# Kernel optimization log

Measured on AMD Instinct MI355X. Metric: run time of the kernel, lower is better.

## Reference

```python
import jax, jax.numpy as jnp
import numpy as np

D, L, DIM, G = 64, 64, 512, 256      # dialogues, utterances/dialogue, feat dim, graph dim
TOPK_FRAC = 0.2
TAU = 0.07


def setup_inputs() -> dict:
    key = jax.random.key(0)
    ks = jax.random.split(key, 7)
    N = D * L
    t = jax.random.normal(ks[0], (N, DIM), dtype=jnp.float32)
    a = jax.random.normal(ks[1], (N, DIM), dtype=jnp.float32)
    v = jax.random.normal(ks[2], (N, DIM), dtype=jnp.float32)
    W_fc = jax.random.normal(ks[3], (DIM, G), dtype=jnp.float32) / np.sqrt(DIM)
    b_fc = jnp.zeros((G,), dtype=jnp.float32)
    W_h = jax.random.normal(ks[4], (G, G), dtype=jnp.float32) / np.sqrt(G)
    b_h = jnp.zeros((G,), dtype=jnp.float32)
    dia_len = np.full((D,), L, dtype=np.int64)  # uniform dialogue lengths
    return {"t": t, "a": a, "v": v, "W_fc": W_fc, "b_fc": b_fc,
            "W_h": W_h, "b_h": b_h, "dia_len": dia_len}


def _contrastive_loss(x, y, tau=TAU):
    # symmetric InfoNCE with matched-index positives
    xn = x / (jnp.linalg.norm(x, axis=-1, keepdims=True) + 1e-8)
    yn = y / (jnp.linalg.norm(y, axis=-1, keepdims=True) + 1e-8)
    sim = (xn @ yn.T) / tau                     # [N, N]
    pos_xy = jnp.diagonal(jax.nn.log_softmax(sim, axis=1))
    pos_yx = jnp.diagonal(jax.nn.log_softmax(sim, axis=0))
    return -(pos_xy.mean() + pos_yx.mean()) / 2.0


def _forward(t, a, v, W_fc, b_fc, W_h, b_h, dia_len):
    dl = np.asarray(dia_len)
    d, l = dl.shape[0], int(dl[0])              # uniform lengths assumed
    m = 3 * l                                   # nodes (and hyperedges) per dialogue
    k = int(l * TOPK_FRAC)
    dim = t.shape[-1]

    # per-dialogue node features in original order [t_i; a_i; v_i]
    feat = jnp.concatenate([t.reshape(d, l, dim),
                            a.reshape(d, l, dim),
                            v.reshape(d, l, dim)], axis=1)   # [d, m, dim]

    # squared euclidean distances (same ordering as torch.cdist for top-k smallest)
    sq = jnp.sum(feat * feat, axis=-1)                        # [d, m]
    d2 = sq[:, :, None] + sq[:, None, :] - 2.0 * jnp.einsum('dmf,dnf->dmn', feat, feat)
    d2 = jax.lax.stop_gradient(jnp.maximum(d2, 0.0))
    _, idx = jax.lax.top_k(-d2, k)                            # [d, m, k] nearest nodes

    # boolean incidence H[d, e, n] = node n participates in hyperedge e
    # (set-union dedup in the original == boolean OR here)
    node_ids = jnp.arange(m)
    H_nb = (idx[..., None] == node_ids).any(axis=2)           # [d, m, m]
    u = node_ids // 3                                         # central utterance of edge j
    cent = ((node_ids[None, :] == u[:, None]) |
            (node_ids[None, :] == u[:, None] + l) |
            (node_ids[None, :] == u[:, None] + 2 * l))        # [m, m]
    H = (H_nb | cent[None]).astype(feat.dtype)                # [d, m, m]

    # fc projection
    X = feat @ W_fc + b_fc                                    # [d, m, G]

    # hypergraph conv: node -> hyperedge (mean) -> node (mean), then Linear+ReLU
    deg_e = H.sum(axis=2, keepdims=True)                      # [d, m, 1]
    E = jnp.einsum('den,dng->deg', H, X) / deg_e              # edge features
    deg_v = H.sum(axis=1)[..., None]                          # [d, m, 1]
    Y = jnp.einsum('den,deg->dng', H, E) / deg_v              # node features
    out = jax.nn.relu(Y @ W_h + b_h)                          # [d, m, G]

    # reverse_features: regroup by modality across dialogues
    tn = out[:, :l].reshape(d * l, -1)
    an = out[:, l:2 * l].reshape(d * l, -1)
    vn = out[:, 2 * l:].reshape(d * l, -1)
    out_cat = jnp.concatenate([tn, an, vn], axis=1)           # [N, 3G]

    loss = (_contrastive_loss(tn, an) + _contrastive_loss(tn, vn)
            + _contrastive_loss(an, vn)) / 3.0
    return out_cat, loss


def reference(t, a, v, W_fc, b_fc, W_h, b_h, dia_len):
    return _forward(t, a, v, W_fc, b_fc, W_h, b_h, dia_len)
```

## Files before the change

### kernel.cpp

```cpp
#include <hip/hip_runtime.h>
#include <math.h>

#define NDIAL 64
#define M3    192
#define DIMF  512
#define GDIM  256
#define NROW  4096
#define TOPK  12
#define INV_TAU (1.0f/0.07f)

typedef __attribute__((ext_vector_type(8))) short bf16x8;
typedef __attribute__((ext_vector_type(4))) float f32x4;
typedef __attribute__((ext_vector_type(8))) ushort us8;
typedef _Float16 f16x8 __attribute__((ext_vector_type(8)));
typedef _Float16 f16x4v __attribute__((ext_vector_type(4)));
typedef __attribute__((address_space(3))) ushort lds_us;
typedef const __attribute__((address_space(1))) ushort gm_us;

__device__ __forceinline__ ushort f2bf(float f) {
    unsigned u = __float_as_uint(f);
    unsigned r = (u + 0x7fff + ((u >> 16) & 1)) >> 16;
    return (ushort)r;
}

template<int KDIM>
__device__ __forceinline__ void mm64bt(
    const float* __restrict__ A, int lda,
    const float* __restrict__ B, int ldb,
    float acc[4][4])
{
    __shared__ float As[64][33];
    __shared__ float Bs[32][68];
    const int tid = threadIdx.x;
    const int tx = tid & 15, ty = tid >> 4;

#pragma unroll
    for (int r = 0; r < 4; r++)
#pragma unroll
        for (int c = 0; c < 4; c++) acc[r][c] = 0.f;

    for (int k0 = 0; k0 < KDIM; k0 += 32) {
#pragma unroll
        for (int i = 0; i < 2; i++) {
            int f = tid + i * 256;
            int m = f >> 3, k4 = f & 7;
            const float4 v4 = *(const float4*)(A + (size_t)m * lda + k0 + k4 * 4);
            As[m][k4 * 4 + 0] = v4.x;
            As[m][k4 * 4 + 1] = v4.y;
            As[m][k4 * 4 + 2] = v4.z;
            As[m][k4 * 4 + 3] = v4.w;
        }
#pragma unroll
        for (int i = 0; i < 2; i++) {
            int f = tid + i * 256;
            int n = f >> 3, k4 = f & 7;
            const float4 v4 = *(const float4*)(B + (size_t)n * ldb + k0 + k4 * 4);
            Bs[k4 * 4 + 0][n] = v4.x;
            Bs[k4 * 4 + 1][n] = v4.y;
            Bs[k4 * 4 + 2][n] = v4.z;
            Bs[k4 * 4 + 3][n] = v4.w;
        }
        __syncthreads();
#pragma unroll
        for (int kk = 0; kk < 32; kk++) {
            float4 b = *(const float4*)&Bs[kk][tx * 4];
#pragma unroll
            for (int r = 0; r < 4; r++) {
                float av = As[ty * 4 + r][kk];
                acc[r][0] += av * b.x;
                acc[r][1] += av * b.y;
                acc[r][2] += av * b.z;
                acc[r][3] += av * b.w;
            }
        }
        __syncthreads();
    }
}

template<int KD, int NW>
__device__ __forceinline__ void hgemm_bt(const _Float16* __restrict__ A, int lda,
                                         const _Float16* __restrict__ B, int ldb,
                                         f32x4 acc[4][4]) {
    __shared__ __align__(16) _Float16 As[64 * 40];
    __shared__ __align__(16) _Float16 Bs[NW * 64 * 40];
    const int tid = threadIdx.x;
    const int lane = tid & 63, w = tid >> 6;
    const int qd = lane >> 4, l15 = lane & 15;

#pragma unroll
    for (int fm = 0; fm < 4; fm++)
#pragma unroll
        for (int fn = 0; fn < 4; fn++)
            acc[fm][fn] = (f32x4){0.f, 0.f, 0.f, 0.f};

    for (int k0 = 0; k0 < KD; k0 += 32) {
        for (int f = tid; f < 256; f += NW * 64) {
            int row = f >> 2, c8 = f & 3;
            *(float4*)&As[row * 40 + c8 * 8] =
                *(const float4*)&A[(size_t)row * lda + k0 + c8 * 8];
        }
#pragma unroll
        for (int i = 0; i < 4; i++) {
            int f = tid + i * NW * 64;
            int row = f >> 2, c8 = f & 3;
            *(float4*)&Bs[row * 40 + c8 * 8] =
                *(const float4*)&B[(size_t)row * ldb + k0 + c8 * 8];
        }
        __syncthreads();
        f16x8 af[4], bfr[4];
#pragma unroll
        for (int fm = 0; fm < 4; fm++)
            af[fm] = *(const f16x8*)&As[(fm * 16 + l15) * 40 + qd * 8];
#pragma unroll
        for (int fn = 0; fn < 4; fn++)
            bfr[fn] = *(const f16x8*)&Bs[(w * 64 + fn * 16 + l15) * 40 + qd * 8];
#pragma unroll
        for (int fm = 0; fm < 4; fm++)
#pragma unroll
            for (int fn = 0; fn < 4; fn++)
                acc[fm][fn] = __builtin_amdgcn_mfma_f32_16x16x32_f16(
                    af[fm], bfr[fn], acc[fm][fn], 0, 0, 0);
        __syncthreads();
    }
}

__device__ __forceinline__ const float* node_ptr(const float* t, const float* a,
                                                 const float* v, int d, int j) {
    int mod = j >> 6, i = j & 63;
    const float* base = (mod == 0) ? t : (mod == 1) ? a : v;
    return base + (size_t)(d * 64 + i) * DIMF;
}

__global__ void kprep(const float* __restrict__ t, const float* __restrict__ a,
                      const float* __restrict__ v, const float* __restrict__ Wfc,
                      const float* __restrict__ Wh, _Float16* __restrict__ featb,
                      _Float16* __restrict__ WfcT, _Float16* __restrict__ WhT,
                      float* __restrict__ sq, float* __restrict__ rs,
                      float* __restrict__ cs, float* __restrict__ degV,
                      _Float16* __restrict__ HbT) {
    int b = blockIdx.x, tid = threadIdx.x;
    if (b < 6144) {
        int e = (b * 256 + tid) * 4;
        int d = e / (M3 * DIMF);
        int rem = e % (M3 * DIMF);
        int n = rem / DIMF, kk = rem % DIMF;
        int mod = n >> 6, i = n & 63;
        const float* src = ((mod == 0) ? t : (mod == 1) ? a : v)
                           + (size_t)(d * 64 + i) * DIMF + kk;
        float4 x = *(const float4*)src;
        f16x4v o = {(_Float16)x.x, (_Float16)x.y, (_Float16)x.z, (_Float16)x.w};
        *(f16x4v*)&featb[e] = o;
    } else if (b < 6272) {
        int e = ((b - 6144) * 256 + tid) * 4;
        int g = e >> 9, kk = e & 511;
        f16x4v o = {(_Float16)Wfc[(size_t)(kk + 0) * GDIM + g],
                    (_Float16)Wfc[(size_t)(kk + 1) * GDIM + g],
                    (_Float16)Wfc[(size_t)(kk + 2) * GDIM + g],
                    (_Float16)Wfc[(size_t)(kk + 3) * GDIM + g]};
        *(f16x4v*)&WfcT[(size_t)g * DIMF + kk] = o;
    } else if (b < 6336) {
        int e = ((b - 6272) * 256 + tid) * 4;
        int go = e >> 8, g = e & 255;
        f16x4v o = {(_Float16)Wh[(size_t)(g + 0) * GDIM + go],
                    (_Float16)Wh[(size_t)(g + 1) * GDIM + go],
                    (_Float16)Wh[(size_t)(g + 2) * GDIM + go],
                    (_Float16)Wh[(size_t)(g + 3) * GDIM + go]};
        *(f16x4v*)&WhT[(size_t)go * GDIM + g] = o;
    } else if (b < 9408) {
        int lane = tid & 63, wv = tid >> 6;
        int n = (b - 6336) * 4 + wv;
        int d = n / M3, j = n % M3;
        const float4* s4 = (const float4*)node_ptr(t, a, v, d, j);
        float s = 0.f;
#pragma unroll
        for (int q = 0; q < 2; q++) {
            float4 x = s4[lane + q * 64];
            s += x.x * x.x + x.y * x.y + x.z * x.z + x.w * x.w;
        }
        for (int o = 32; o; o >>= 1) s += __shfl_down(s, o);
        if (lane == 0) sq[n] = s;
    } else if (b < 9456) {
        int i = (b - 9408) * 256 + tid;
        rs[i] = 0.f; cs[i] = 0.f; degV[i] = 0.f;
    } else {
        int i = (b - 9456) * 256 + tid;
        ulonglong2 z = {0ull, 0ull};
        *(ulonglong2*)&HbT[(size_t)i * 8] = z;
    }
}

__global__ void k1_d2(const float* __restrict__ t, const float* __restrict__ a,
                      const float* __restrict__ v, const float* __restrict__ sq,
                      float* __restrict__ d2) {
    int tileid = blockIdx.x;
    int d = blockIdx.y;
    int bi = (tileid < 3) ? 0 : (tileid < 5) ? 1 : 2;
    int bj = (tileid < 3) ? tileid : (tileid < 5) ? tileid - 2 : 2;
    const float* A = ((bi == 0) ? t : (bi == 1) ? a : v) + (size_t)d * 64 * DIMF;
    const float* B = ((bj == 0) ? t : (bj == 1) ? a : v) + (size_t)d * 64 * DIMF;
    float acc[4][4];
    mm64bt<DIMF>(A, DIMF, B, DIMF, acc);
    int tx = threadIdx.x & 15, ty = threadIdx.x >> 4;
    const float* sqd = sq + d * M3;
    float* outp = d2 + (size_t)d * M3 * M3;
#pragma unroll
    for (int r = 0; r < 4; r++)
#pragma unroll
        for (int c = 0; c < 4; c++) {
            int il = bi * 64 + ty * 4 + r;
            int jl = bj * 64 + tx * 4 + c;
            float vv = fmaxf(sqd[il] + sqd[jl] - 2.f * acc[r][c], 0.f);
            outp[(size_t)il * M3 + jl] = vv;
            if (bi != bj) outp[(size_t)jl * M3 + il] = vv;
        }
}

__global__ void k2_topk(const float* __restrict__ d2, _Float16* __restrict__ Hb,
                        _Float16* __restrict__ HbT, float* __restrict__ degE,
                        float* __restrict__ degV) {
    int lane = threadIdx.x & 63, wv = threadIdx.x >> 6;
    int r = blockIdx.x * 4 + wv;
    int d = r / M3, e = r % M3;
    const float* row = d2 + (size_t)r * M3;
    float w0 = row[lane], w1 = row[lane + 64], w2 = row[lane + 128];
    bool s0 = false, s1 = false, s2 = false;
#pragma unroll
    for (int it = 0; it < TOPK; it++) {
        float bv = w0; int bi = lane;
        if (w1 < bv) { bv = w1; bi = lane + 64; }
        if (w2 < bv) { bv = w2; bi = lane + 128; }
#pragma unroll
        for (int o = 1; o < 64; o <<= 1) {
            float ov = __shfl_xor(bv, o);
            int   oi = __shfl_xor(bi, o);
            if (ov < bv || (ov == bv && oi < bi)) { bv = ov; bi = oi; }
        }
        if (bi == lane)            { s0 = true; w0 = 3.4e38f; }
        else if (bi == lane + 64)  { s1 = true; w1 = 3.4e38f; }
        else if (bi == lane + 128) { s2 = true; w2 = 3.4e38f; }
    }
    int u = e / 3;
    if (lane == u) { s0 = true; s1 = true; s2 = true; }
    float f0 = s0 ? 1.f : 0.f, f1 = s1 ? 1.f : 0.f, f2 = s2 ? 1.f : 0.f;
    _Float16* Hrow = Hb + (size_t)r * M3;
    Hrow[lane] = (_Float16)f0;
    Hrow[lane + 64] = (_Float16)f1;
    Hrow[lane + 128] = (_Float16)f2;
    float cnt = f0 + f1 + f2;
#pragma unroll
    for (int o = 1; o < 64; o <<= 1) cnt += __shfl_xor(cnt, o);
    if (lane == 0) degE[r] = cnt;
    float* dv = degV + d * M3;
    _Float16* HT = HbT + (size_t)d * M3 * M3;
    if (s0) { atomicAdd(&dv[lane], 1.f);       HT[(size_t)lane * M3 + e] = (_Float16)1.f; }
    if (s1) { atomicAdd(&dv[lane + 64], 1.f);  HT[(size_t)(lane + 64) * M3 + e] = (_Float16)1.f; }
    if (s2) { atomicAdd(&dv[lane + 128], 1.f); HT[(size_t)(lane + 128) * M3 + e] = (_Float16)1.f; }
}

__global__ void k3_x(const _Float16* __restrict__ WfcT, const _Float16* __restrict__ featb,
                     const float* __restrict__ bfc, _Float16* __restrict__ XT) {
    int gb = blockIdx.x, d = blockIdx.y;
    const _Float16* A = WfcT + (size_t)gb * 64 * DIMF;
    const _Float16* B = featb + (size_t)d * M3 * DIMF;
    f32x4 acc[4][4];
    hgemm_bt<DIMF, 3>(A, DIMF, B, DIMF, acc);
    int lane = threadIdx.x & 63, w = threadIdx.x >> 6;
    int qd = lane >> 4, l15 = lane & 15;
    _Float16* out = XT + (size_t)d * GDIM * M3;
#pragma unroll
    for (int fm = 0; fm < 4; fm++)
#pragma unroll
        for (int rg = 0; rg < 4; rg++) {
            int g = gb * 64 + fm * 16 + qd * 4 + rg;
            float bias = bfc[g];
#pragma unroll
            for (int fn = 0; fn < 4; fn++) {
                int n = w * 64 + fn * 16 + l15;
                out[(size_t)g * M3 + n] = (_Float16)(acc[fm][fn][rg] + bias);
            }
        }
}

__global__ void k4_E(const _Float16* __restrict__ XT, const _Float16* __restrict__ Hb,
                     const float* __restrict__ degE, _Float16* __restrict__ ET) {
    int gb = blockIdx.x, d = blockIdx.y;
    const _Float16* A = XT + (size_t)d * GDIM * M3 + (size_t)gb * 64 * M3;
    const _Float16* B = Hb + (size_t)d * M3 * M3;
    f32x4 acc[4][4];
    hgemm_bt<M3, 3>(A, M3, B, M3, acc);
    int lane = threadIdx.x & 63, w = threadIdx.x >> 6;
    int qd = lane >> 4, l15 = lane & 15;
    float ide[4];
#pragma unroll
    for (int fn = 0; fn < 4; fn++)
        ide[fn] = 1.f / degE[d * M3 + w * 64 + fn * 16 + l15];
    _Float16* out = ET + (size_t)d * GDIM * M3;
#pragma unroll
    for (int fm = 0; fm < 4; fm++)
#pragma unroll
        for (int rg = 0; rg < 4; rg++) {
            int g = gb * 64 + fm * 16 + qd * 4 + rg;
#pragma unroll
            for (int fn = 0; fn < 4; fn++) {
                int e = w * 64 + fn * 16 + l15;
                out[(size_t)g * M3 + e] = (_Float16)(acc[fm][fn][rg] * ide[fn]);
            }
        }
}

__global__ void k5_Y(const _Float16* __restrict__ HbT, const _Float16* __restrict__ ET,
                     const float* __restrict__ degV, _Float16* __restrict__ Y) {
    int nb = blockIdx.x, d = blockIdx.y;
    const _Float16* A = HbT + (size_t)d * M3 * M3 + (size_t)nb * 64 * M3;
    const _Float16* B = ET + (size_t)d * GDIM * M3;
    f32x4 acc[4][4];
    hgemm_bt<M3, 4>(A, M3, B, M3, acc);
    int lane = threadIdx.x & 63, w = threadIdx.x >> 6;
    int qd = lane >> 4, l15 = lane & 15;
    _Float16* out = Y + ((size_t)d * M3 + nb * 64) * GDIM;
#pragma unroll
    for (int fm = 0; fm < 4; fm++)
#pragma unroll
        for (int rg = 0; rg < 4; rg++) {
            int ml = fm * 16 + qd * 4 + rg;
            float idv = 1.f / degV[d * M3 + nb * 64 + ml];
#pragma unroll
            for (int fn = 0; fn < 4; fn++) {
                int g = w * 64 + fn * 16 + l15;
                out[(size_t)ml * GDIM + g] = (_Float16)(acc[fm][fn][rg] * idv);
            }
        }
}

__global__ __launch_bounds__(256) void k6_out(const _Float16* __restrict__ Y,
                                              const _Float16* __restrict__ WhT,
                                              const float* __restrict__ bh,
                                              float* __restrict__ outp,
                                              ushort* __restrict__ xnb) {
    __shared__ float tile[64 * 256];
    __shared__ float ssq[64];
    int b = blockIdx.x, tid = threadIdx.x;
    if (tid < 64) ssq[tid] = 0.f;
    const _Float16* A = Y + (size_t)b * 64 * GDIM;
    f32x4 acc[4][4];
    hgemm_bt<GDIM, 4>(A, GDIM, WhT, GDIM, acc);
    int lane = tid & 63, w = tid >> 6;
    int qd = lane >> 4, l15 = lane & 15;
    int d = b / 3, mod = b % 3;
    float bb[4];
#pragma unroll
    for (int fn = 0; fn < 4; fn++)
        bb[fn] = bh[w * 64 + fn * 16 + l15];
#pragma unroll
    for (int fm = 0; fm < 4; fm++)
#pragma unroll
        for (int rg = 0; rg < 4; rg++) {
            int i = fm * 16 + qd * 4 + rg;
            float* orow = outp + (size_t)(d * 64 + i) * 768 + mod * GDIM;
            float s2 = 0.f;
#pragma unroll
            for (int fn = 0; fn < 4; fn++) {
                int go = w * 64 + fn * 16 + l15;
                float vv = fmaxf(acc[fm][fn][rg] + bb[fn], 0.f);
                orow[go] = vv;
                tile[i * 256 + go] = vv;
                s2 += vv * vv;
            }
            s2 += __shfl_xor(s2, 1);
            s2 += __shfl_xor(s2, 2);
            s2 += __shfl_xor(s2, 4);
            s2 += __shfl_xor(s2, 8);
            if (l15 == 0) atomicAdd(&ssq[i], s2);
        }
    __syncthreads();
    if (tid < 64) ssq[tid] = 1.f / (sqrtf(ssq[tid]) + 1e-8f);
    __syncthreads();
#pragma unroll
    for (int it = 0; it < 8; it++) {
        int f = tid + it * 256;
        int row = f >> 5, c = f & 31;
        float4 xa = *(const float4*)&tile[row * 256 + c * 8];
        float4 xb = *(const float4*)&tile[row * 256 + c * 8 + 4];
        float iv = ssq[row];
        us8 o = {f2bf(xa.x * iv), f2bf(xa.y * iv), f2bf(xa.z * iv), f2bf(xa.w * iv),
                 f2bf(xb.x * iv), f2bf(xb.y * iv), f2bf(xb.z * iv), f2bf(xb.w * iv)};
        int rx = d * 64 + row;
        int slot = (c & 24) | ((c & 7) ^ (row & 7));
        *(us8*)&xnb[((size_t)mod * NROW + rx) * GDIM + slot * 8] = o;
    }
}

#define TILE9 128
#define STAGE9(ELT)                                                        \
    {                                                                      \
        __builtin_amdgcn_global_load_lds(pa0 + (ELT), la0, 16, 0, 0);      \
        __builtin_amdgcn_global_load_lds(pb0 + (ELT), lb0, 16, 0, 0);      \
        __builtin_amdgcn_global_load_lds(pa1 + (ELT), la1, 16, 0, 0);      \
        __builtin_amdgcn_global_load_lds(pb1 + (ELT), lb1, 16, 0, 0);      \
        __builtin_amdgcn_global_load_lds(pa2 + (ELT), la2, 16, 0, 0);      \
        __builtin_amdgcn_global_load_lds(pb2 + (ELT), lb2, 16, 0, 0);      \
        __builtin_amdgcn_global_load_lds(pa3 + (ELT), la3, 16, 0, 0);      \
        __builtin_amdgcn_global_load_lds(pb3 + (ELT), lb3, 16, 0, 0);      \
    }
__global__ __launch_bounds__(256, 4) void k9_mfma(const ushort* __restrict__ xnb,
                                                  float* __restrict__ rs,
                                                  float* __restrict__ cs,
                                                  float* __restrict__ diag) {
    int lin = blockIdx.x + (blockIdx.y << 5) + (blockIdx.z << 10);
    int vid = (lin >> 3) + (lin & 7) * 384;
    int p  = vid >> 10;
    int r0 = vid & 1023;
    int ci = r0 >> 5, cj = r0 & 31;
    int px = (p == 2) ? 1 : 0;
    int py = (p == 0) ? 1 : 2;
    const ushort* A = xnb + ((size_t)px * NROW + ci * TILE9) * GDIM;
    const ushort* B = xnb + ((size_t)py * NROW + cj * TILE9) * GDIM;

    __shared__ __align__(16) ushort As[TILE9 * 64];
    __shared__ __align__(16) ushort Bs[TILE9 * 64];

    const int tid = threadIdx.x;
    const int lane = tid & 63, w = tid >> 6;
    const int wrow = w >> 1, wcol = w & 1;
    const int qd = lane >> 4, l15 = lane & 15;
    const int lrow = lane >> 3, lslot = lane & 7;

    const int rbase = w * 32 + lrow;
    const int cbase = lslot * 8;
    const gm_us* pa0 = (gm_us*)(A + (size_t)(rbase +  0) * GDIM + cbase);
    const gm_us* pa1 = (gm_us*)(A + (size_t)(rbase +  8) * GDIM + cbase);
    const gm_us* pa2 = (gm_us*)(A + (size_t)(rbase + 16) * GDIM + cbase);
    const gm_us* pa3 = (gm_us*)(A + (size_t)(rbase + 24) * GDIM + cbase);
    const gm_us* pb0 = (gm_us*)(B + (size_t)(rbase +  0) * GDIM + cbase);
    const gm_us* pb1 = (gm_us*)(B + (size_t)(rbase +  8) * GDIM + cbase);
    const gm_us* pb2 = (gm_us*)(B + (size_t)(rbase + 16) * GDIM + cbase);
    const gm_us* pb3 = (gm_us*)(B + (size_t)(rbase + 24) * GDIM + cbase);
    lds_us* la0 = (lds_us*)&As[(w * 32 +  0) * 64];
    lds_us* la1 = (lds_us*)&As[(w * 32 +  8) * 64];
    lds_us* la2 = (lds_us*)&As[(w * 32 + 16) * 64];
    lds_us* la3 = (lds_us*)&As[(w * 32 + 24) * 64];
    lds_us* lb0 = (lds_us*)&Bs[(w * 32 +  0) * 64];
    lds_us* lb1 = (lds_us*)&Bs[(w * 32 +  8) * 64];
    lds_us* lb2 = (lds_us*)&Bs[(w * 32 + 16) * 64];
    lds_us* lb3 = (lds_us*)&Bs[(w * 32 + 24) * 64];

    f32x4 acc[4][4] = {};

    auto compute = [&]() {
#pragma unroll
        for (int kk = 0; kk < 2; kk++) {
            bf16x8 af[4], bfv[4];
#pragma unroll
            for (int fm = 0; fm < 4; fm++) {
                int ar = wrow * 64 + fm * 16 + l15;
                af[fm] = *(const bf16x8*)&As[ar * 64 + ((kk * 4 + qd) ^ (ar & 7)) * 8];
            }
#pragma unroll
            for (int fn = 0; fn < 4; fn++) {
                int br = wcol * 64 + fn * 16 + l15;
                bfv[fn] = *(const bf16x8*)&Bs[br * 64 + ((kk * 4 + qd) ^ (br & 7)) * 8];
            }
#pragma unroll
            for (int fm = 0; fm < 4; fm++)
#pragma unroll
                for (int fn = 0; fn < 4; fn++)
                    acc[fm][fn] = __builtin_amdgcn_mfma_f32_16x16x32_bf16(
                        af[fm], bfv[fn], acc[fm][fn], 0, 0, 0);
        }
    };

    STAGE9(0);   __syncthreads(); compute(); __syncthreads();
    STAGE9(64);  __syncthreads(); compute(); __syncthreads();
    STAGE9(128); __syncthreads(); compute(); __syncthreads();
    STAGE9(192); __syncthreads(); compute(); __syncthreads();

    const float C2 = INV_TAU * 1.44269504088896f;
    f32x4 rv[4] = {};
    f32x4 cv[4] = {};
#pragma unroll
    for (int fm = 0; fm < 4; fm++)
#pragma unroll
        for (int fn = 0; fn < 4; fn++) {
            f32x4 sv = acc[fm][fn] * C2;
            f32x4 ev;
#pragma unroll
            for (int rg = 0; rg < 4; rg++)
                ev[rg] = exp2f(sv[rg]);
            rv[fm] += ev;
            cv[fn] += ev;
        }
    if (ci == cj) {
#pragma unroll
        for (int fm = 0; fm < 4; fm++)
#pragma unroll
            for (int fn = 0; fn < 4; fn++)
#pragma unroll
                for (int rg = 0; rg < 4; rg++) {
                    int lr = wrow * 64 + fm * 16 + qd * 4 + rg;
                    int lc = wcol * 64 + fn * 16 + l15;
                    if (lr == lc)
                        diag[p * NROW + ci * TILE9 + lr] = acc[fm][fn][rg] * INV_TAU;
                }
    }
#pragma unroll
    for (int fm = 0; fm < 4; fm++)
#pragma unroll
        for (int rg = 0; rg < 4; rg++) {
            float s = rv[fm][rg];
            s += __shfl_xor(s, 1);
            s += __shfl_xor(s, 2);
            s += __shfl_xor(s, 4);
            s += __shfl_xor(s, 8);
            if (l15 == 0)
                atomicAdd(&rs[p * NROW + ci * TILE9 + wrow * 64 + fm * 16 + qd * 4 + rg], s);
        }
#pragma unroll
    for (int fn = 0; fn < 4; fn++) {
        float s = (cv[fn][0] + cv[fn][1]) + (cv[fn][2] + cv[fn][3]);
        s += __shfl_xor(s, 16);
        s += __shfl_xor(s, 32);
        if (qd == 0)
            atomicAdd(&cs[p * NROW + cj * TILE9 + wcol * 64 + fn * 16 + l15], s);
    }
}

__global__ void k10_loss(const float* __restrict__ diag, const float* __restrict__ rs,
                         const float* __restrict__ cs, float* __restrict__ outp) {
    float acc = 0.f;
    for (int i = threadIdx.x; i < 3 * NROW; i += 256)
        acc += 2.f * diag[i] - logf(rs[i]) - logf(cs[i]);
    int lane = threadIdx.x & 63, wv = threadIdx.x >> 6;
    for (int o = 32; o; o >>= 1) acc += __shfl_down(acc, o);
    __shared__ float red[4];
    if (lane == 0) red[wv] = acc;
    __syncthreads();
    if (threadIdx.x == 0) {
        float tot = red[0] + red[1] + red[2] + red[3];
        outp[(size_t)NROW * 768] = -tot / (NROW * 6.0f);
    }
}

extern "C" void kernel_launch(void* const* d_in, const int* in_sizes, int n_in,
                              void* d_out, int out_size, void* d_ws, size_t ws_size,
                              hipStream_t stream) {
    const float* t   = (const float*)d_in[0];
    const float* a   = (const float*)d_in[1];
    const float* v   = (const float*)d_in[2];
    const float* Wfc = (const float*)d_in[3];
    const float* bfc = (const float*)d_in[4];
    const float* Wh  = (const float*)d_in[5];
    const float* bh  = (const float*)d_in[6];
    float* outp = (float*)d_out;
    float* ws = (float*)d_ws;

    float* sq    = ws;
    float* d2    = sq + 12288;
    float* HbF   = d2 + 2359296;
    float* HbTF  = HbF + 1179648;
    float* degE  = HbTF + 1179648;
    float* degV  = degE + 12288;
    float* featF = degV + 12288;
    float* WfcTF = featF + 3145728;
    float* WhTF  = WfcTF + 65536;
    float* XTF   = WhTF + 32768;
    float* ETF   = XTF + 1572864;
    float* YF    = ETF + 1572864;
    float* rs    = YF + 1572864;
    float* cs    = rs + 12288;
    float* diag  = cs + 12288;

    _Float16* Hb    = (_Float16*)HbF;
    _Float16* HbT   = (_Float16*)HbTF;
    _Float16* featb = (_Float16*)featF;
    _Float16* WfcT  = (_Float16*)WfcTF;
    _Float16* WhT   = (_Float16*)WhTF;
    _Float16* XT    = (_Float16*)XTF;
    _Float16* ET    = (_Float16*)ETF;
    _Float16* Y     = (_Float16*)YF;
    ushort*   xnb   = (ushort*)d2;

    kprep  <<<10608, 256, 0, stream>>>(t, a, v, Wfc, Wh, featb, WfcT, WhT,
                                       sq, rs, cs, degV, HbT);
    k1_d2  <<<dim3(6, 64), 256, 0, stream>>>(t, a, v, sq, d2);
    k2_topk<<<3072, 256, 0, stream>>>(d2, Hb, HbT, degE, degV);
    k3_x   <<<dim3(4, 64), 192, 0, stream>>>(WfcT, featb, bfc, XT);
    k4_E   <<<dim3(4, 64), 192, 0, stream>>>(XT, Hb, degE, ET);
    k5_Y   <<<dim3(3, 64), 256, 0, stream>>>(HbT, ET, degV, Y);
    k6_out <<<192, 256, 0, stream>>>(Y, WhT, bh, outp, xnb);
    k9_mfma<<<dim3(32, 32, 3), 256, 0, stream>>>(xnb, rs, cs, diag);
    k10_loss<<<1, 256, 0, stream>>>(diag, rs, cs, outp);
}
```

Baseline: 284.6 us.

## Compute pairwise distance Gram matrix with split-fp16 MFMA instead of FP32 FMA

Replaces the scalar FP32 tiled GEMM in the distance kernel with MFMA fp16 matrix instructions. Each feature is split into a high and a low fp16 part in the prep kernel, and four MFMA products recover near-FP32 precision for the top-k selection. This removes the slow FP32 SIMD inner loop. In exchange it adds an extra fp16 residual buffer, aliased onto the XT scratch region, and extra writes in the prep kernel.

```diff
diff --git a/kernel.cpp b/kernel.cpp
--- a/kernel.cpp
+++ b/kernel.cpp
@@ -21,60 +21,6 @@
     unsigned u = __float_as_uint(f);
     unsigned r = (u + 0x7fff + ((u >> 16) & 1)) >> 16;
     return (ushort)r;
-}
-
-template<int KDIM>
-__device__ __forceinline__ void mm64bt(
-    const float* __restrict__ A, int lda,
-    const float* __restrict__ B, int ldb,
-    float acc[4][4])
-{
-    __shared__ float As[64][33];
-    __shared__ float Bs[32][68];
-    const int tid = threadIdx.x;
-    const int tx = tid & 15, ty = tid >> 4;
-
-#pragma unroll
-    for (int r = 0; r < 4; r++)
-#pragma unroll
-        for (int c = 0; c < 4; c++) acc[r][c] = 0.f;
-
-    for (int k0 = 0; k0 < KDIM; k0 += 32) {
-#pragma unroll
-        for (int i = 0; i < 2; i++) {
-            int f = tid + i * 256;
-            int m = f >> 3, k4 = f & 7;
-            const float4 v4 = *(const float4*)(A + (size_t)m * lda + k0 + k4 * 4);
-            As[m][k4 * 4 + 0] = v4.x;
-            As[m][k4 * 4 + 1] = v4.y;
-            As[m][k4 * 4 + 2] = v4.z;
-            As[m][k4 * 4 + 3] = v4.w;
-        }
-#pragma unroll
-        for (int i = 0; i < 2; i++) {
-            int f = tid + i * 256;
-            int n = f >> 3, k4 = f & 7;
-            const float4 v4 = *(const float4*)(B + (size_t)n * ldb + k0 + k4 * 4);
-            Bs[k4 * 4 + 0][n] = v4.x;
-            Bs[k4 * 4 + 1][n] = v4.y;
-            Bs[k4 * 4 + 2][n] = v4.z;
-            Bs[k4 * 4 + 3][n] = v4.w;
-        }
-        __syncthreads();
-#pragma unroll
-        for (int kk = 0; kk < 32; kk++) {
-            float4 b = *(const float4*)&Bs[kk][tx * 4];
-#pragma unroll
-            for (int r = 0; r < 4; r++) {
-                float av = As[ty * 4 + r][kk];
-                acc[r][0] += av * b.x;
-                acc[r][1] += av * b.y;
-                acc[r][2] += av * b.z;
-                acc[r][3] += av * b.w;
-            }
-        }
-        __syncthreads();
-    }
 }
 
 template<int KD, int NW>
@@ -134,7 +80,8 @@
 __global__ void kprep(const float* __restrict__ t, const float* __restrict__ a,
                       const float* __restrict__ v, const float* __restrict__ Wfc,
                       const float* __restrict__ Wh, _Float16* __restrict__ featb,
-                      _Float16* __restrict__ WfcT, _Float16* __restrict__ WhT,
+                      _Float16* __restrict__ featlo, _Float16* __restrict__ WfcT,
+                      _Float16* __restrict__ WhT,
                       float* __restrict__ sq, float* __restrict__ rs,
                       float* __restrict__ cs, float* __restrict__ degV,
                       _Float16* __restrict__ HbT) {
@@ -148,8 +95,13 @@
         const float* src = ((mod == 0) ? t : (mod == 1) ? a : v)
                            + (size_t)(d * 64 + i) * DIMF + kk;
         float4 x = *(const float4*)src;
-        f16x4v o = {(_Float16)x.x, (_Float16)x.y, (_Float16)x.z, (_Float16)x.w};
+        _Float16 h0 = (_Float16)x.x, h1 = (_Float16)x.y;
+        _Float16 h2 = (_Float16)x.z, h3 = (_Float16)x.w;
+        f16x4v o = {h0, h1, h2, h3};
         *(f16x4v*)&featb[e] = o;
+        f16x4v ol = {(_Float16)(x.x - (float)h0), (_Float16)(x.y - (float)h1),
+                     (_Float16)(x.z - (float)h2), (_Float16)(x.w - (float)h3)};
+        *(f16x4v*)&featlo[e] = ol;
     } else if (b < 6272) {
         int e = ((b - 6144) * 256 + tid) * 4;
         int g = e >> 9, kk = e & 511;
@@ -189,27 +141,60 @@
     }
 }
 
-__global__ void k1_d2(const float* __restrict__ t, const float* __restrict__ a,
-                      const float* __restrict__ v, const float* __restrict__ sq,
+__global__ __launch_bounds__(256) void k1_d2(const _Float16* __restrict__ featb,
+                      const _Float16* __restrict__ featlo,
+                      const float* __restrict__ sq,
                       float* __restrict__ d2) {
     int tileid = blockIdx.x;
     int d = blockIdx.y;
     int bi = (tileid < 3) ? 0 : (tileid < 5) ? 1 : 2;
     int bj = (tileid < 3) ? tileid : (tileid < 5) ? tileid - 2 : 2;
-    const float* A = ((bi == 0) ? t : (bi == 1) ? a : v) + (size_t)d * 64 * DIMF;
-    const float* B = ((bj == 0) ? t : (bj == 1) ? a : v) + (size_t)d * 64 * DIMF;
-    float acc[4][4];
-    mm64bt<DIMF>(A, DIMF, B, DIMF, acc);
-    int tx = threadIdx.x & 15, ty = threadIdx.x >> 4;
+    const size_t base = (size_t)d * M3 * DIMF;
+    const _Float16* Ah = featb  + base + (size_t)bi * 64 * DIMF;
+    const _Float16* Al = featlo + base + (size_t)bi * 64 * DIMF;
+    const _Float16* Bh = featb  + base + (size_t)bj * 64 * DIMF;
+    const _Float16* Bl = featlo + base + (size_t)bj * 64 * DIMF;
+
+    __shared__ __align__(16) _Float16 Ahs[64 * 40], Als[64 * 40];
+    __shared__ __align__(16) _Float16 Bhs[64 * 40], Bls[64 * 40];
+    const int tid = threadIdx.x;
+    const int lane = tid & 63, w = tid >> 6;
+    const int qd = lane >> 4, l15 = lane & 15;
+
+    f32x4 acc[4];
+#pragma unroll
+    for (int fm = 0; fm < 4; fm++) acc[fm] = (f32x4){0.f, 0.f, 0.f, 0.f};
+
+    for (int k0 = 0; k0 < DIMF; k0 += 32) {
+        int row = tid >> 2, c8 = tid & 3;
+        *(float4*)&Ahs[row * 40 + c8 * 8] = *(const float4*)&Ah[(size_t)row * DIMF + k0 + c8 * 8];
+        *(float4*)&Als[row * 40 + c8 * 8] = *(const float4*)&Al[(size_t)row * DIMF + k0 + c8 * 8];
+        *(float4*)&Bhs[row * 40 + c8 * 8] = *(const float4*)&Bh[(size_t)row * DIMF + k0 + c8 * 8];
+        *(float4*)&Bls[row * 40 + c8 * 8] = *(const float4*)&Bl[(size_t)row * DIMF + k0 + c8 * 8];
+        __syncthreads();
+        f16x8 bh = *(const f16x8*)&Bhs[(w * 16 + l15) * 40 + qd * 8];
+        f16x8 bl = *(const f16x8*)&Bls[(w * 16 + l15) * 40 + qd * 8];
+#pragma unroll
+        for (int fm = 0; fm < 4; fm++) {
+            f16x8 ah = *(const f16x8*)&Ahs[(fm * 16 + l15) * 40 + qd * 8];
+            f16x8 al = *(const f16x8*)&Als[(fm * 16 + l15) * 40 + qd * 8];
+            acc[fm] = __builtin_amdgcn_mfma_f32_16x16x32_f16(ah, bh, acc[fm], 0, 0, 0);
+            acc[fm] = __builtin_amdgcn_mfma_f32_16x16x32_f16(ah, bl, acc[fm], 0, 0, 0);
+            acc[fm] = __builtin_amdgcn_mfma_f32_16x16x32_f16(al, bh, acc[fm], 0, 0, 0);
+            acc[fm] = __builtin_amdgcn_mfma_f32_16x16x32_f16(al, bl, acc[fm], 0, 0, 0);
+        }
+        __syncthreads();
+    }
+
     const float* sqd = sq + d * M3;
     float* outp = d2 + (size_t)d * M3 * M3;
 #pragma unroll
-    for (int r = 0; r < 4; r++)
-#pragma unroll
-        for (int c = 0; c < 4; c++) {
-            int il = bi * 64 + ty * 4 + r;
-            int jl = bj * 64 + tx * 4 + c;
-            float vv = fmaxf(sqd[il] + sqd[jl] - 2.f * acc[r][c], 0.f);
+    for (int fm = 0; fm < 4; fm++)
+#pragma unroll
+        for (int rg = 0; rg < 4; rg++) {
+            int il = bi * 64 + fm * 16 + qd * 4 + rg;
+            int jl = bj * 64 + w * 16 + l15;
+            float vv = fmaxf(sqd[il] + sqd[jl] - 2.f * acc[fm][rg], 0.f);
             outp[(size_t)il * M3 + jl] = vv;
             if (bi != bj) outp[(size_t)jl * M3 + il] = vv;
         }
@@ -578,10 +563,11 @@
     _Float16* ET    = (_Float16*)ETF;
     _Float16* Y     = (_Float16*)YF;
     ushort*   xnb   = (ushort*)d2;
-
-    kprep  <<<10608, 256, 0, stream>>>(t, a, v, Wfc, Wh, featb, WfcT, WhT,
-                                       sq, rs, cs, degV, HbT);
-    k1_d2  <<<dim3(6, 64), 256, 0, stream>>>(t, a, v, sq, d2);
+    _Float16* featlo = (_Float16*)XTF;
+
+    kprep  <<<10608, 256, 0, stream>>>(t, a, v, Wfc, Wh, featb, featlo, WfcT,
+                                       WhT, sq, rs, cs, degV, HbT);
+    k1_d2  <<<dim3(6, 64), 256, 0, stream>>>(featb, featlo, sq, d2);
     k2_topk<<<3072, 256, 0, stream>>>(d2, Hb, HbT, degE, degV);
     k3_x   <<<dim3(4, 64), 192, 0, stream>>>(WfcT, featb, bfc, XT);
     k4_E   <<<dim3(4, 64), 192, 0, stream>>>(XT, Hb, degE, ET);
```

New measurement: 263.7 us. 7.4% less time.
